# Optimization experiments

Measured on AMD Instinct MI355X. Metric: run time of the kernel, lower is better.

The kernel has to match this reference:

```python
import jax, jax.numpy as jnp
import numpy as np

EPS = 1e-9
P, Dp, D, Dd, ITERS = 6, 8, 4, 12, 2


def squash(v, axis=-1):
    s2 = jnp.sum(v * v, axis=axis, keepdims=True)
    return s2 / (1.0 + s2) * v / (jnp.sqrt(s2) + EPS)


def setup_inputs() -> dict:
    key = jax.random.key(0)
    kx, kwp, kw = jax.random.split(key, 3)
    B, L, C, K = 64, 1024, 128, 6
    X = jax.random.normal(kx, (B, L, C, K), dtype=jnp.float32)
    # primary linear: Linear(C -> P*Dp)
    Wp = jax.random.normal(kwp, (P * Dp, C), dtype=jnp.float32) * (1.0 / np.sqrt(C))
    bp = jnp.zeros((P * Dp,), dtype=jnp.float32)
    # routing weights W: [K, D, Dd, P*Dp], xavier-uniform scale
    lim = np.sqrt(6.0 / (Dd + P * Dp))
    W = jax.random.uniform(kw, (K, D, Dd, P * Dp), dtype=jnp.float32, minval=-lim, maxval=lim)
    return {"X": X, "Wp": Wp, "bp": bp, "W": W}


def reference(X, Wp, bp, W):
    B, L, C, K = X.shape
    # primary projection: [B,L,K,C] @ [C, P*Dp]
    Xk = jnp.transpose(X, (0, 1, 3, 2))            # [B,L,K,C]
    Xp = jnp.einsum('blkc,pc->blkp', Xk, Wp) + bp   # [B,L,K,P*Dp]
    Xp = squash(Xp.reshape(B, L, K, P, Dp), axis=-1).reshape(B, L, K, P * Dp)
    # prediction vectors u_hat: [B,L,K,D,Dd]
    u_hat = jnp.einsum('kdqp,blkp->blkdq', W, Xp)
    # dynamic routing
    b = jnp.zeros((B, L, K, D), dtype=X.dtype)
    v = None
    for _ in range(ITERS):
        c = jax.nn.softmax(b, axis=-1)                     # over D
        s = jnp.einsum('blkd,blkdq->bldq', c, u_hat)       # sum over K
        v = squash(s, axis=-1)                             # [B,L,D,Dd]
        b = b + jnp.einsum('blkdq,bldq->blkd', u_hat, v)
    return v.reshape(B, L, D * Dd)
```

## Files before the change

kernel.cpp:

```cpp
#include <hip/hip_runtime.h>
#include <hip/hip_bf16.h>
#include <math.h>

#define EPSQ 1e-9f

typedef float  floatx4 __attribute__((ext_vector_type(4)));
typedef short  short8  __attribute__((ext_vector_type(8)));
typedef unsigned short u16;
typedef unsigned int   u32;

constexpr int TP  = 16;
constexpr int SA  = 40;
constexpr int SS  = 52;
constexpr int SA2 = 40;

__device__ __forceinline__ void cvt_hilo(float a, float b, u32& hi, u32& lo) {
    __hip_bfloat162 h = __float22bfloat162_rn(make_float2(a, b));
    float2 hf = __bfloat1622float2(h);
    __hip_bfloat162 l = __float22bfloat162_rn(make_float2(a - hf.x, b - hf.y));
    __builtin_memcpy(&hi, &h, 4);
    __builtin_memcpy(&lo, &l, 4);
}

__device__ __forceinline__ float g16sum(float x) {
    x += __shfl_xor(x, 1);
    x += __shfl_xor(x, 2);
    x += __shfl_xor(x, 4);
    x += __shfl_xor(x, 8);
    return x;
}

__device__ __forceinline__ void route_and_write(float u0, float u1, float u2,
                                                float u3, float u4, float u5,
                                                int d, int q, bool act,
                                                float* __restrict__ out, long pos)
{
    float s = (u0 + u1 + u2 + u3 + u4 + u5) * 0.25f;
    float s2 = g16sum(s * s);
    float v = s * (s2 / (1.0f + s2) / (sqrtf(s2) + EPSQ));

    float ss = 0.f;
#define ROUTE_K(UK)                                        \
    {                                                      \
        float b = g16sum((UK) * v);                        \
        float mm = fmaxf(b, __shfl_xor(b, 16));            \
        mm = fmaxf(mm, __shfl_xor(mm, 32));                \
        float e = __expf(b - mm);                          \
        float es = e + __shfl_xor(e, 16);                  \
        es += __shfl_xor(es, 32);                          \
        ss = fmaf(e / es, (UK), ss);                       \
    }
    ROUTE_K(u0) ROUTE_K(u1) ROUTE_K(u2) ROUTE_K(u3) ROUTE_K(u4) ROUTE_K(u5)
#undef ROUTE_K
    float ss2 = g16sum(ss * ss);
    float vv = ss * (ss2 / (1.0f + ss2) / (sqrtf(ss2) + EPSQ));
    if (act) out[pos * 48 + d * 12 + q] = vv;
}

__global__ void prep_kernel(const float* __restrict__ Wp, const float* __restrict__ W,
                            u16* __restrict__ wpf, u16* __restrict__ wf) {
    int gid = blockIdx.x * 256 + threadIdx.x;
    int stride = gridDim.x * 256;
    for (int i = gid; i < 12288; i += stride) {
        int j = i & 7, lane = (i >> 3) & 63, kc = (i >> 9) & 3, vt = i >> 11;
        int var = (vt >= 3) ? 1 : 0;
        int ct = vt - 3 * var;
        int p = ct * 16 + (lane & 15);
        int c = kc * 32 + (lane >> 4) * 8 + j;
        float x = Wp[p * 128 + c];
        __hip_bfloat16 hb = __float2bfloat16(x);
        if (var) { float hf = __bfloat162float(hb); hb = __float2bfloat16(x - hf); }
        u16 u; __builtin_memcpy(&u, &hb, 2);
        wpf[i] = u;
    }
    for (int i = gid; i < 36864; i += stride) {
        int j = i & 7, lane = (i >> 3) & 63, kc = (i >> 9) & 1, q3 = i >> 10;
        int ct = q3 % 3, kk = q3 / 3;
        int k = kk % 6, var = kk / 6;
        int dq = ct * 16 + (lane & 15);
        int p = kc * 32 + (lane >> 4) * 8 + j;
        float x = (p < 48) ? W[(k * 48 + dq) * 48 + p] : 0.f;
        __hip_bfloat16 hb = __float2bfloat16(x);
        if (var) { float hf = __bfloat162float(hb); hb = __float2bfloat16(x - hf); }
        u16 u; __builtin_memcpy(&u, &hb, 2);
        wf[i] = u;
    }
}

__global__ __launch_bounds__(256)
void capsule_kernel(
    const float* __restrict__ X,
    const float* __restrict__ bp,
    const u16* __restrict__ wpf,
    const u16* __restrict__ wf,
    float* __restrict__ out)
{
    __shared__ __align__(16) char raw[19968 + 2 * 96 * SA2 * 2];
    float* sS   = (float*)raw;
    float* sU   = (float*)raw;
    u16*  sAh   = (u16*)raw;
    u16*  sAl   = sAh + 96 * SA;
    u16*  sA2h  = (u16*)(raw + 19968);
    u16*  sA2l  = sA2h + 96 * SA2;

    const int t    = threadIdx.x;
    const int lane = t & 63;
    const int w    = t >> 6;
    const int m    = lane & 15;
    const int quad = lane >> 4;
    const long pos_base = (long)blockIdx.x * TP;

    floatx4 acc_a = {0.f,0.f,0.f,0.f}, acc_b = {0.f,0.f,0.f,0.f}, acc_c = {0.f,0.f,0.f,0.f},
            acc_d = {0.f,0.f,0.f,0.f}, acc_e = {0.f,0.f,0.f,0.f};

#define S1_TILE(ACC, TI)                                                              \
    { int T = w + 4 * (TI);                                                           \
      if (T < 18) {                                                                   \
        int rt = T / 3, ct = T - 3 * rt;                                              \
        short8 ah = *(const short8*)(sAh + (rt * 16 + m) * SA + quad * 8);            \
        short8 al = *(const short8*)(sAl + (rt * 16 + m) * SA + quad * 8);            \
        short8 bh = *(const short8*)(wpf + ((ct * 4 + kc) * 64 + lane) * 8);          \
        short8 bl = *(const short8*)(wpf + (((3 + ct) * 4 + kc) * 64 + lane) * 8);    \
        ACC = __builtin_amdgcn_mfma_f32_16x16x32_bf16(ah, bh, ACC, 0, 0, 0);          \
        ACC = __builtin_amdgcn_mfma_f32_16x16x32_bf16(ah, bl, ACC, 0, 0, 0);          \
        ACC = __builtin_amdgcn_mfma_f32_16x16x32_bf16(al, bh, ACC, 0, 0, 0);          \
      } }

    #pragma unroll
    for (int kc = 0; kc < 4; ++kc) {
        if (kc > 0) __syncthreads();
        {
            int pos = t >> 4, cp = t & 15;
            const float4* src = (const float4*)(X + (pos_base + pos) * 768 + kc * 192) + cp * 3;
            float4 f0 = src[0], f1 = src[1], f2 = src[2];
            u16* bh = sAh + (pos * 6) * SA + cp * 2;
            u16* bl = sAl + (pos * 6) * SA + cp * 2;
            u32 h, l;
            cvt_hilo(f0.x, f1.z, h, l); *(u32*)(bh + 0 * SA) = h; *(u32*)(bl + 0 * SA) = l;
            cvt_hilo(f0.y, f1.w, h, l); *(u32*)(bh + 1 * SA) = h; *(u32*)(bl + 1 * SA) = l;
            cvt_hilo(f0.z, f2.x, h, l); *(u32*)(bh + 2 * SA) = h; *(u32*)(bl + 2 * SA) = l;
            cvt_hilo(f0.w, f2.y, h, l); *(u32*)(bh + 3 * SA) = h; *(u32*)(bl + 3 * SA) = l;
            cvt_hilo(f1.x, f2.z, h, l); *(u32*)(bh + 4 * SA) = h; *(u32*)(bl + 4 * SA) = l;
            cvt_hilo(f1.y, f2.w, h, l); *(u32*)(bh + 5 * SA) = h; *(u32*)(bl + 5 * SA) = l;
        }
        __syncthreads();
        S1_TILE(acc_a, 0) S1_TILE(acc_b, 1) S1_TILE(acc_c, 2) S1_TILE(acc_d, 3) S1_TILE(acc_e, 4)
    }
#undef S1_TILE
    __syncthreads();

#define S1_EPI(ACC, TI)                                                   \
    { int T = w + 4 * (TI);                                               \
      if (T < 18) {                                                       \
        int rt = T / 3, ct = T - 3 * rt;                                  \
        float b = bp[ct * 16 + m];                                        \
        float* dst = sS + (rt * 16 + quad * 4) * SS + ct * 16 + m;        \
        dst[0 * SS] = ACC.x + b; dst[1 * SS] = ACC.y + b;                 \
        dst[2 * SS] = ACC.z + b; dst[3 * SS] = ACC.w + b;                 \
      } }
    S1_EPI(acc_a, 0) S1_EPI(acc_b, 1) S1_EPI(acc_c, 2) S1_EPI(acc_d, 3) S1_EPI(acc_e, 4)
#undef S1_EPI
    __syncthreads();

    for (int g = t; g < 576; g += 256) {
        int row = g / 6, grp = g - 6 * row;
        float* p = sS + row * SS + grp * 8;
        float4 v0 = *(float4*)p;
        float4 v1 = *(float4*)(p + 4);
        float s2 = v0.x * v0.x + v0.y * v0.y + v0.z * v0.z + v0.w * v0.w
                 + v1.x * v1.x + v1.y * v1.y + v1.z * v1.z + v1.w * v1.w;
        float r = s2 / (1.0f + s2) / (sqrtf(s2) + EPSQ);
        v0.x *= r; v0.y *= r; v0.z *= r; v0.w *= r;
        v1.x *= r; v1.y *= r; v1.z *= r; v1.w *= r;
        *(float4*)p = v0;
        *(float4*)(p + 4) = v1;
    }
    __syncthreads();

    floatx4 uacc_a = {0.f,0.f,0.f,0.f}, uacc_b = {0.f,0.f,0.f,0.f}, uacc_c = {0.f,0.f,0.f,0.f},
            uacc_d = {0.f,0.f,0.f,0.f}, uacc_e = {0.f,0.f,0.f,0.f};

#define S2_TILE(ACC, TI)                                                                    \
    { int T = w + 4 * (TI);                                                                 \
      if (T < 18) {                                                                         \
        int k = T / 3, ct = T - 3 * k;                                                      \
        short8 ah = *(const short8*)(sA2h + (k * 16 + m) * SA2 + quad * 8);                 \
        short8 al = *(const short8*)(sA2l + (k * 16 + m) * SA2 + quad * 8);                 \
        short8 bh = *(const short8*)(wf + (((k * 3 + ct) * 2 + kc2) * 64 + lane) * 8);      \
        short8 bl = *(const short8*)(wf + ((((6 + k) * 3 + ct) * 2 + kc2) * 64 + lane) * 8);\
        ACC = __builtin_amdgcn_mfma_f32_16x16x32_bf16(ah, bh, ACC, 0, 0, 0);                \
        ACC = __builtin_amdgcn_mfma_f32_16x16x32_bf16(ah, bl, ACC, 0, 0, 0);                \
        ACC = __builtin_amdgcn_mfma_f32_16x16x32_bf16(al, bh, ACC, 0, 0, 0);                \
      } }

    #pragma unroll
    for (int kc2 = 0; kc2 < 2; ++kc2) {
        if (kc2 > 0) __syncthreads();
        if (t < 192) {
            int rowA2 = t >> 1, half = t & 1;
            int pos = rowA2 & 15, k = rowA2 >> 4;
            int rowS = pos * 6 + k;
            u16* dh = sA2h + rowA2 * SA2 + half * 16;
            u16* dl = sA2l + rowA2 * SA2 + half * 16;
            if (kc2 == 0 || half == 0) {
                const float4* s = (const float4*)(sS + rowS * SS + kc2 * 32 + half * 16);
                #pragma unroll
                for (int g = 0; g < 4; ++g) {
                    float4 v = s[g];
                    u32 h0, l0, h1, l1;
                    cvt_hilo(v.x, v.y, h0, l0);
                    cvt_hilo(v.z, v.w, h1, l1);
                    *(u32*)(dh + g * 4)     = h0; *(u32*)(dh + g * 4 + 2) = h1;
                    *(u32*)(dl + g * 4)     = l0; *(u32*)(dl + g * 4 + 2) = l1;
                }
            } else {
                #pragma unroll
                for (int g = 0; g < 4; ++g) {
                    *(u32*)(dh + g * 4) = 0u; *(u32*)(dh + g * 4 + 2) = 0u;
                    *(u32*)(dl + g * 4) = 0u; *(u32*)(dl + g * 4 + 2) = 0u;
                }
            }
        }
        __syncthreads();
        S2_TILE(uacc_a, 0) S2_TILE(uacc_b, 1) S2_TILE(uacc_c, 2) S2_TILE(uacc_d, 3) S2_TILE(uacc_e, 4)
    }
#undef S2_TILE

#define S2_EPI(ACC, TI)                                                   \
    { int T = w + 4 * (TI);                                               \
      if (T < 18) {                                                       \
        int k = T / 3, ct = T - 3 * k;                                    \
        sU[((quad * 4 + 0) * 6 + k) * SS + ct * 16 + m] = ACC.x;          \
        sU[((quad * 4 + 1) * 6 + k) * SS + ct * 16 + m] = ACC.y;          \
        sU[((quad * 4 + 2) * 6 + k) * SS + ct * 16 + m] = ACC.z;          \
        sU[((quad * 4 + 3) * 6 + k) * SS + ct * 16 + m] = ACC.w;          \
      } }
    S2_EPI(uacc_a, 0) S2_EPI(uacc_b, 1) S2_EPI(uacc_c, 2) S2_EPI(uacc_d, 3) S2_EPI(uacc_e, 4)
#undef S2_EPI
    __syncthreads();

    const int d = lane >> 4;
    const int q = lane & 15;
    const bool act = (q < 12);
    const int dqi = d * 12 + (act ? q : 0);

    #pragma unroll
    for (int i = 0; i < 4; ++i) {
        int pos = w * 4 + i;
        const float* u = sU + (pos * 6) * SS + dqi;
        float a0 = u[0 * SS], a1 = u[1 * SS], a2 = u[2 * SS];
        float a3 = u[3 * SS], a4 = u[4 * SS], a5 = u[5 * SS];
        if (!act) { a0 = a1 = a2 = a3 = a4 = a5 = 0.f; }
        route_and_write(a0, a1, a2, a3, a4, a5, d, q, act, out, pos_base + pos);
    }
}

extern "C" void kernel_launch(void* const* d_in, const int* in_sizes, int n_in,
                              void* d_out, int out_size, void* d_ws, size_t ws_size,
                              hipStream_t stream) {
    const float* X  = (const float*)d_in[0];
    const float* Wp = (const float*)d_in[1];
    const float* bp = (const float*)d_in[2];
    const float* W  = (const float*)d_in[3];
    float* out = (float*)d_out;

    u16* wpf = (u16*)d_ws;
    u16* wf  = wpf + 12288;

    hipLaunchKernelGGL(prep_kernel, dim3(48), dim3(256), 0, stream, Wp, W, wpf, wf);

    const int n_pos = 64 * 1024;
    hipLaunchKernelGGL(capsule_kernel, dim3(n_pos / TP), dim3(256), 0, stream,
                       X, bp, wpf, wf, out);
}
```

Before: 339.7 us.

## Fuse primary bias+squash+bf16 split into MFMA epilogue, drop fp32 staging

The stage-1 accumulators now get bias added, are squashed with an 8-lane shuffle reduction, split into bf16 hi/lo and written straight into the stage-2 A operand in shared memory. This removes the fp32 staging buffer, one squash pass and the per-chunk conversion loop, along with several barriers. Stage 2 now issues both K chunks back to back, reading a zero pad for the unused upper half. Shared memory shrinks and launch bounds ask for 8 blocks per CU to raise occupancy, at the cost of stricter register limits and scattered 16-bit LDS stores.

Measured after the change: 354.6 us. 1.04x slower.

```diff
diff --git a/kernel.cpp b/kernel.cpp
--- a/kernel.cpp
+++ b/kernel.cpp
@@ -11,8 +11,9 @@
 
 constexpr int TP  = 16;
 constexpr int SA  = 40;
-constexpr int SS  = 52;
-constexpr int SA2 = 40;
+constexpr int SS  = 49;
+constexpr int SA2 = 48;
+
 
 __device__ __forceinline__ void cvt_hilo(float a, float b, u32& hi, u32& lo) {
     __hip_bfloat162 h = __float22bfloat162_rn(make_float2(a, b));
@@ -27,6 +28,13 @@
     x += __shfl_xor(x, 2);
     x += __shfl_xor(x, 4);
     x += __shfl_xor(x, 8);
+    return x;
+}
+
+__device__ __forceinline__ float g8sum(float x) {
+    x += __shfl_xor(x, 1);
+    x += __shfl_xor(x, 2);
+    x += __shfl_xor(x, 4);
     return x;
 }
 
@@ -87,7 +95,7 @@
     }
 }
 
-__global__ __launch_bounds__(256)
+__global__ __launch_bounds__(256, 8)
 void capsule_kernel(
     const float* __restrict__ X,
     const float* __restrict__ bp,
@@ -95,13 +103,13 @@
     const u16* __restrict__ wf,
     float* __restrict__ out)
 {
-    __shared__ __align__(16) char raw[19968 + 2 * 96 * SA2 * 2];
-    float* sS   = (float*)raw;
+    __shared__ __align__(16) char raw[18848];
+    u16*   sAh  = (u16*)raw;
+    u16*   sAl  = sAh + 96 * SA;
+    u16*   sA2h = (u16*)raw;
+    u16*   sA2l = sA2h + 96 * SA2;
     float* sU   = (float*)raw;
-    u16*  sAh   = (u16*)raw;
-    u16*  sAl   = sAh + 96 * SA;
-    u16*  sA2h  = (u16*)(raw + 19968);
-    u16*  sA2l  = sA2h + 96 * SA2;
+    const u16* zpad = (const u16*)(raw + 18816);
 
     const int t    = threadIdx.x;
     const int lane = t & 63;
@@ -109,6 +117,8 @@
     const int m    = lane & 15;
     const int quad = lane >> 4;
     const long pos_base = (long)blockIdx.x * TP;
+
+    if (t < 8) ((u32*)(raw + 18816))[t] = 0u;
 
     floatx4 acc_a = {0.f,0.f,0.f,0.f}, acc_b = {0.f,0.f,0.f,0.f}, acc_c = {0.f,0.f,0.f,0.f},
             acc_d = {0.f,0.f,0.f,0.f}, acc_e = {0.f,0.f,0.f,0.f};
@@ -149,32 +159,37 @@
 #undef S1_TILE
     __syncthreads();
 
-#define S1_EPI(ACC, TI)                                                   \
-    { int T = w + 4 * (TI);                                               \
-      if (T < 18) {                                                       \
-        int rt = T / 3, ct = T - 3 * rt;                                  \
-        float b = bp[ct * 16 + m];                                        \
-        float* dst = sS + (rt * 16 + quad * 4) * SS + ct * 16 + m;        \
-        dst[0 * SS] = ACC.x + b; dst[1 * SS] = ACC.y + b;                 \
-        dst[2 * SS] = ACC.z + b; dst[3 * SS] = ACC.w + b;                 \
-      } }
-    S1_EPI(acc_a, 0) S1_EPI(acc_b, 1) S1_EPI(acc_c, 2) S1_EPI(acc_d, 3) S1_EPI(acc_e, 4)
-#undef S1_EPI
-    __syncthreads();
-
-    for (int g = t; g < 576; g += 256) {
-        int row = g / 6, grp = g - 6 * row;
-        float* p = sS + row * SS + grp * 8;
-        float4 v0 = *(float4*)p;
-        float4 v1 = *(float4*)(p + 4);
-        float s2 = v0.x * v0.x + v0.y * v0.y + v0.z * v0.z + v0.w * v0.w
-                 + v1.x * v1.x + v1.y * v1.y + v1.z * v1.z + v1.w * v1.w;
-        float r = s2 / (1.0f + s2) / (sqrtf(s2) + EPSQ);
-        v0.x *= r; v0.y *= r; v0.z *= r; v0.w *= r;
-        v1.x *= r; v1.y *= r; v1.z *= r; v1.w *= r;
-        *(float4*)p = v0;
-        *(float4*)(p + 4) = v1;
-    }
+#define FUSE_ONE(V)                                                   \
+    { float val = (V) + bv;                                           \
+      float s2 = g8sum(val * val);                                    \
+      float rf = s2 / (1.0f + s2) / (sqrtf(s2) + EPSQ);               \
+      float sv = val * rf;                                            \
+      __hip_bfloat16 hb = __float2bfloat16(sv);                       \
+      float hf = __bfloat162float(hb);                                \
+      __hip_bfloat16 lb = __float2bfloat16(sv - hf);                  \
+      u16 hu, lu;                                                     \
+      __builtin_memcpy(&hu, &hb, 2); __builtin_memcpy(&lu, &lb, 2);   \
+      int dr = (kk * 16 + pp) * SA2 + ct * 16 + m;                    \
+      sA2h[dr] = hu; sA2l[dr] = lu; }
+
+#define S1_FUSE(ACC, TI)                                              \
+    { int T = w + 4 * (TI);                                           \
+      if (T < 18) {                                                   \
+        int rt = T / 3, ct = T - 3 * rt;                              \
+        float bv = bp[ct * 16 + m];                                   \
+        int row0 = rt * 16 + quad * 4;                                \
+        int pp = row0 / 6, kk = row0 - 6 * pp;                        \
+        FUSE_ONE(ACC.x)                                               \
+        kk++; if (kk == 6) { kk = 0; pp++; }                          \
+        FUSE_ONE(ACC.y)                                               \
+        kk++; if (kk == 6) { kk = 0; pp++; }                          \
+        FUSE_ONE(ACC.z)                                               \
+        kk++; if (kk == 6) { kk = 0; pp++; }                          \
+        FUSE_ONE(ACC.w)                                               \
+      } }
+    S1_FUSE(acc_a, 0) S1_FUSE(acc_b, 1) S1_FUSE(acc_c, 2) S1_FUSE(acc_d, 3) S1_FUSE(acc_e, 4)
+#undef S1_FUSE
+#undef FUSE_ONE
     __syncthreads();
 
     floatx4 uacc_a = {0.f,0.f,0.f,0.f}, uacc_b = {0.f,0.f,0.f,0.f}, uacc_c = {0.f,0.f,0.f,0.f},
@@ -184,47 +199,28 @@
     { int T = w + 4 * (TI);                                                                 \
       if (T < 18) {                                                                         \
         int k = T / 3, ct = T - 3 * k;                                                      \
-        short8 ah = *(const short8*)(sA2h + (k * 16 + m) * SA2 + quad * 8);                 \
-        short8 al = *(const short8*)(sA2l + (k * 16 + m) * SA2 + quad * 8);                 \
-        short8 bh = *(const short8*)(wf + (((k * 3 + ct) * 2 + kc2) * 64 + lane) * 8);      \
-        short8 bl = *(const short8*)(wf + ((((6 + k) * 3 + ct) * 2 + kc2) * 64 + lane) * 8);\
-        ACC = __builtin_amdgcn_mfma_f32_16x16x32_bf16(ah, bh, ACC, 0, 0, 0);                \
-        ACC = __builtin_amdgcn_mfma_f32_16x16x32_bf16(ah, bl, ACC, 0, 0, 0);                \
-        ACC = __builtin_amdgcn_mfma_f32_16x16x32_bf16(al, bh, ACC, 0, 0, 0);                \
-      } }
-
-    #pragma unroll
-    for (int kc2 = 0; kc2 < 2; ++kc2) {
-        if (kc2 > 0) __syncthreads();
-        if (t < 192) {
-            int rowA2 = t >> 1, half = t & 1;
-            int pos = rowA2 & 15, k = rowA2 >> 4;
-            int rowS = pos * 6 + k;
-            u16* dh = sA2h + rowA2 * SA2 + half * 16;
-            u16* dl = sA2l + rowA2 * SA2 + half * 16;
-            if (kc2 == 0 || half == 0) {
-                const float4* s = (const float4*)(sS + rowS * SS + kc2 * 32 + half * 16);
-                #pragma unroll
-                for (int g = 0; g < 4; ++g) {
-                    float4 v = s[g];
-                    u32 h0, l0, h1, l1;
-                    cvt_hilo(v.x, v.y, h0, l0);
-                    cvt_hilo(v.z, v.w, h1, l1);
-                    *(u32*)(dh + g * 4)     = h0; *(u32*)(dh + g * 4 + 2) = h1;
-                    *(u32*)(dl + g * 4)     = l0; *(u32*)(dl + g * 4 + 2) = l1;
-                }
-            } else {
-                #pragma unroll
-                for (int g = 0; g < 4; ++g) {
-                    *(u32*)(dh + g * 4) = 0u; *(u32*)(dh + g * 4 + 2) = 0u;
-                    *(u32*)(dl + g * 4) = 0u; *(u32*)(dl + g * 4 + 2) = 0u;
-                }
-            }
-        }
-        __syncthreads();
-        S2_TILE(uacc_a, 0) S2_TILE(uacc_b, 1) S2_TILE(uacc_c, 2) S2_TILE(uacc_d, 3) S2_TILE(uacc_e, 4)
-    }
+        const u16* arh = sA2h + (k * 16 + m) * SA2;                                         \
+        const u16* arl = sA2l + (k * 16 + m) * SA2;                                         \
+        short8 ah0 = *(const short8*)(arh + quad * 8);                                      \
+        short8 al0 = *(const short8*)(arl + quad * 8);                                      \
+        const u16* a1h = (quad < 2) ? (arh + 32 + quad * 8) : zpad;                         \
+        const u16* a1l = (quad < 2) ? (arl + 32 + quad * 8) : zpad;                         \
+        short8 ah1 = *(const short8*)a1h;                                                   \
+        short8 al1 = *(const short8*)a1l;                                                   \
+        short8 bh0 = *(const short8*)(wf + (((k * 3 + ct) * 2 + 0) * 64 + lane) * 8);       \
+        short8 bl0 = *(const short8*)(wf + ((((6 + k) * 3 + ct) * 2 + 0) * 64 + lane) * 8); \
+        short8 bh1 = *(const short8*)(wf + (((k * 3 + ct) * 2 + 1) * 64 + lane) * 8);       \
+        short8 bl1 = *(const short8*)(wf + ((((6 + k) * 3 + ct) * 2 + 1) * 64 + lane) * 8); \
+        ACC = __builtin_amdgcn_mfma_f32_16x16x32_bf16(ah0, bh0, ACC, 0, 0, 0);              \
+        ACC = __builtin_amdgcn_mfma_f32_16x16x32_bf16(ah0, bl0, ACC, 0, 0, 0);              \
+        ACC = __builtin_amdgcn_mfma_f32_16x16x32_bf16(al0, bh0, ACC, 0, 0, 0);              \
+        ACC = __builtin_amdgcn_mfma_f32_16x16x32_bf16(ah1, bh1, ACC, 0, 0, 0);              \
+        ACC = __builtin_amdgcn_mfma_f32_16x16x32_bf16(ah1, bl1, ACC, 0, 0, 0);              \
+        ACC = __builtin_amdgcn_mfma_f32_16x16x32_bf16(al1, bh1, ACC, 0, 0, 0);              \
+      } }
+    S2_TILE(uacc_a, 0) S2_TILE(uacc_b, 1) S2_TILE(uacc_c, 2) S2_TILE(uacc_d, 3) S2_TILE(uacc_e, 4)
 #undef S2_TILE
+    __syncthreads();
 
 #define S2_EPI(ACC, TI)                                                   \
     { int T = w + 4 * (TI);                                               \
```
